# Kernel optimization log

Measured on AMD Instinct MI355X. Metric: run time of the kernel, lower is better.

Reference implementation:

```python
import jax, jax.numpy as jnp
import numpy as np

GAMMA = 1.0
MAX_SIMILARITY = 1.0


def setup_inputs() -> dict:
    key = jax.random.key(0)
    k1, k2 = jax.random.split(key)
    B, Ns, D = 128, 512, 256
    d_vectors = jax.random.normal(k1, (B, Ns, D), dtype=jnp.float32)
    # Normalized similarity matrix (MinMaxScaler output lies in [0, 1])
    S = jax.random.uniform(k2, (Ns, Ns), dtype=jnp.float32)
    return {"d_vectors": d_vectors, "S": S}


def reference(d_vectors, S):
    B, Ns, D = d_vectors.shape
    eye = jnp.eye(Ns, dtype=d_vectors.dtype)

    # Pairwise squared distances: ||di||^2 + ||dj||^2 - 2 di.dj  -> [B, Ns, Ns]
    n2 = jnp.sum(d_vectors * d_vectors, axis=-1)  # [B, Ns]
    sq = n2[:, :, None] + n2[:, None, :] - 2.0 * jnp.einsum("bid,bjd->bij", d_vectors, d_vectors)
    sq = jnp.maximum(sq, 0.0) * (1.0 - eye)  # exact zero on the diagonal

    # Safe sqrt (subgradient 0 at zero distance, matching torch.norm)
    dist = jnp.where(sq > 0, jnp.sqrt(jnp.where(sq > 0, sq, 1.0)), 0.0)
    Kd = jnp.exp(-GAMMA * dist)  # Gaussian-kernel Gram matrix [B, Ns, Ns]

    # Norm-ratio loss
    W = (S > 0).astype(d_vectors.dtype)  # [Ns, Ns]
    denom = jnp.linalg.norm(W - eye)  # Frobenius norm, scalar
    Kd_tilde = Kd * (1.0 - eye)  # zero diagonal
    S_tilde = S - MAX_SIMILARITY * eye
    diff = W * (Kd_tilde - S_tilde)  # broadcast over batch
    numer = jnp.sqrt(jnp.sum(diff * diff, axis=(1, 2)))  # [B]
    losses = 2.0 * numer / denom
    return jnp.sum(losses)
```

## Files before the change

### kernel.cpp

```cpp
#include <hip/hip_runtime.h>
#include <hip/hip_bf16.h>

typedef __bf16 bf16_t;
typedef __bf16 bf16x4 __attribute__((ext_vector_type(4)));
typedef __bf16 bf16x8 __attribute__((ext_vector_type(8)));
typedef float f32x4 __attribute__((ext_vector_type(4)));
typedef float f32x16 __attribute__((ext_vector_type(16)));
typedef long i64x2 __attribute__((ext_vector_type(2)));
typedef int i32x4 __attribute__((ext_vector_type(4)));

#define BATCH 128
#define NS 512
#define DIM 256
#define BT 128
#define NT 10
#define LDSP 272
#define CSTRIDE 132

__global__ __launch_bounds__(256) void prep_st_kernel(const float* __restrict__ dv,
                                                      const float* __restrict__ S,
                                                      unsigned char* __restrict__ f8,
                                                      float* __restrict__ n2g,
                                                      float* __restrict__ St,
                                                      float* __restrict__ dpartial) {
    const int bidx = blockIdx.x;
    const int t = threadIdx.x;
    if (bidx < 256) {
        const int bi = bidx >> 4, bj = bidx & 15;
        const int c  = t & 31, r0 = t >> 5;
        __shared__ float tileS[32][33];
        __shared__ float red[4];
        float dacc = 0.0f;
#pragma unroll
        for (int k = 0; k < 4; ++k) {
            const int r  = r0 + k * 8;
            const int gi = bi * 32 + r, gj = bj * 32 + c;
            const float s = S[(size_t)gi * NS + gj];
            tileS[r][c] = s;
            const float w = (s > 0.0f) ? 1.0f : 0.0f;
            const float e = (gi == gj) ? 1.0f : 0.0f;
            const float d = w - e;
            dacc += d * d;
        }
        __syncthreads();
#pragma unroll
        for (int k = 0; k < 4; ++k) {
            const int r = r0 + k * 8;
            St[(size_t)(bj * 32 + r) * NS + bi * 32 + c] = tileS[c][r];
        }
        const int lane = t & 63, wave = t >> 6;
#pragma unroll
        for (int off = 32; off >= 1; off >>= 1) dacc += __shfl_down(dacc, off, 64);
        if (lane == 0) red[wave] = dacc;
        __syncthreads();
        if (t == 0) dpartial[bidx] = red[0] + red[1] + red[2] + red[3];
    } else {
        const int wid  = ((bidx - 256) << 2) | (t >> 6);
        const int lane = t & 63;
#pragma unroll
        for (int it = 0; it < 8; ++it) {
            const int row = wid + it * 8192;
            const f32x4 v = *reinterpret_cast<const f32x4*>(dv + (size_t)row * DIM + lane * 4);
            float pn = v[0]*v[0] + v[1]*v[1] + v[2]*v[2] + v[3]*v[3];
#pragma unroll
            for (int off = 32; off >= 1; off >>= 1) pn += __shfl_xor(pn, off, 64);
            int w0 = __builtin_amdgcn_cvt_pk_fp8_f32(v[0], v[1], 0, false);
            w0     = __builtin_amdgcn_cvt_pk_fp8_f32(v[2], v[3], w0, true);
            *reinterpret_cast<int*>(f8 + (size_t)row * DIM + lane * 4) = w0;
            if (lane == 0) n2g[row] = pn;
        }
    }
}

__global__ __launch_bounds__(512, 4) void gram_pair_kernel(const unsigned char* __restrict__ f8,
                                                           const float* __restrict__ n2g,
                                                           const float* __restrict__ S,
                                                           const float* __restrict__ St,
                                                           float* __restrict__ partial) {
    const int bid  = blockIdx.x;
    const int work = (bid & 7) * 160 + (bid >> 3);
    const int b    = work / NT;
    const int idx  = work - b * NT;
    int ti, tj;
    if (idx < 4)      { ti = 0; tj = idx; }
    else if (idx < 7) { ti = 1; tj = idx - 3; }
    else if (idx < 9) { ti = 2; tj = idx - 5; }
    else              { ti = 3; tj = 3; }
    const bool diag = (ti == tj);
    const int t    = threadIdx.x;
    const int wave = t >> 6, lane = t & 63;
    const int wr   = wave >> 2, wc = wave & 3;
    const int col  = lane & 31, kh = lane >> 5;

    __shared__ __attribute__((aligned(16))) char smem[256 * LDSP];
    __shared__ float n2s[256];
    __shared__ float red[8];
    char*  sP = smem;
    float* sC = reinterpret_cast<float*>(smem);

    {
        const int g     = t >> 8;
        const int tg    = t & 255;
        const int off16 = (tg & 15) * 16;
        const int rbase = tg >> 4;
        if (g == 0 || !diag) {
            const int psel = g ? tj : ti;
            const unsigned char* src = f8 + ((size_t)b * NS + (size_t)psel * BT) * DIM;
#pragma unroll
            for (int it = 0; it < 8; ++it) {
                const int row = it * 16 + rbase;
                const i32x4 v = *reinterpret_cast<const i32x4*>(src + (size_t)row * DIM + off16);
                *reinterpret_cast<i32x4*>(&sP[(g * 128 + row) * LDSP + off16]) = v;
            }
        }
        if (t < 256) {
            const int p = t >> 7;
            if (p == 0 || !diag) {
                const int psel2 = p ? tj : ti;
                n2s[t] = n2g[(size_t)b * NS + (size_t)psel2 * BT + (t & 127)];
            }
        }
    }
    __syncthreads();

    const int boff = diag ? 0 : 128;
    const char* aP = &sP[(wr * 64 + col) * LDSP + kh * 16];
    const char* bP = &sP[(boff + wc * 32 + col) * LDSP + kh * 16];
    f32x16 acc0 = (f32x16)(0.0f);
    f32x16 acc1 = (f32x16)(0.0f);
    __builtin_amdgcn_s_setprio(1);
#pragma unroll
    for (int u = 0; u < 8; ++u) {
        const i64x2 A0 = *reinterpret_cast<const i64x2*>(aP + u * 32);
        const i64x2 A1 = *reinterpret_cast<const i64x2*>(aP + 32 * LDSP + u * 32);
        const i64x2 Bv = *reinterpret_cast<const i64x2*>(bP + u * 32);
        acc0 = __builtin_amdgcn_mfma_f32_32x32x16_fp8_fp8(A0[0], Bv[0], acc0, 0, 0, 0);
        acc1 = __builtin_amdgcn_mfma_f32_32x32x16_fp8_fp8(A1[0], Bv[0], acc1, 0, 0, 0);
        acc0 = __builtin_amdgcn_mfma_f32_32x32x16_fp8_fp8(A0[1], Bv[1], acc0, 0, 0, 0);
        acc1 = __builtin_amdgcn_mfma_f32_32x32x16_fp8_fp8(A1[1], Bv[1], acc1, 0, 0, 0);
    }
    __builtin_amdgcn_s_setprio(0);
    __syncthreads();

    {
        const int lj = wc * 32 + col;
        const float n2j = n2s[boff + lj];
#pragma unroll
        for (int m = 0; m < 2; ++m) {
            const f32x16 av = m ? acc1 : acc0;
#pragma unroll
            for (int h4 = 0; h4 < 4; ++h4) {
#pragma unroll
                for (int e = 0; e < 4; ++e) {
                    const int li = wr * 64 + m * 32 + h4 * 8 + kh * 4 + e;
                    const float c = av[h4 * 4 + e];
                    const float sq = fmaxf(n2s[li] + n2j - 2.0f * c, 0.0f);
                    sC[li * CSTRIDE + lj] = __expf(-__builtin_amdgcn_sqrtf(sq));
                }
            }
        }
    }
    __syncthreads();

    float local = 0.0f;
    {
        const int rg = t >> 4;
        const int ln = t & 15;
        f32x4 s1a[8], s2a[8];
#pragma unroll
        for (int it = 0; it < 8; ++it) {
            const int li  = rg + (it >> 1) * 32;
            const int ljb = (it & 1) * 64 + ln * 4;
            const int gi  = ti * BT + li;
            s1a[it] = *reinterpret_cast<const f32x4*>(S  + (size_t)gi * NS + tj * BT + ljb);
            s2a[it] = diag ? (f32x4)(0.0f)
                           : *reinterpret_cast<const f32x4*>(St + (size_t)gi * NS + tj * BT + ljb);
        }
#pragma unroll
        for (int it = 0; it < 8; ++it) {
            const int li  = rg + (it >> 1) * 32;
            const int ljb = (it & 1) * 64 + ln * 4;
            const f32x4 kdv = *reinterpret_cast<const f32x4*>(&sC[li * CSTRIDE + ljb]);
#pragma unroll
            for (int e = 0; e < 4; ++e) {
                const int lj = ljb + e;
                const float kd = kdv[e];
                const float s1 = s1a[it][e];
                if (diag) {
                    float d = (li == lj) ? (1.0f - s1) : (kd - s1);
                    d *= (s1 > 0.0f) ? 1.0f : 0.0f;
                    local += d * d;
                } else {
                    const float s2 = s2a[it][e];
                    const float d1 = (s1 > 0.0f) ? (kd - s1) : 0.0f;
                    const float d2 = (s2 > 0.0f) ? (kd - s2) : 0.0f;
                    local += d1 * d1 + d2 * d2;
                }
            }
        }
    }

#pragma unroll
    for (int off = 32; off >= 1; off >>= 1) local += __shfl_down(local, off, 64);
    if (lane == 0) red[wave] = local;
    __syncthreads();
    if (t == 0) {
        float s = 0.0f;
#pragma unroll
        for (int w = 0; w < 8; ++w) s += red[w];
        partial[(size_t)b * NT + idx] = s;
    }
}


__global__ __launch_bounds__(256) void norms_kernel(const float* __restrict__ dv,
                                                    float* __restrict__ n2) {
    const int row  = blockIdx.x * 4 + (threadIdx.x >> 6);
    const int lane = threadIdx.x & 63;
    const float4 v = *reinterpret_cast<const float4*>(dv + (size_t)row * DIM + lane * 4);
    float s = v.x * v.x + v.y * v.y + v.z * v.z + v.w * v.w;
#pragma unroll
    for (int off = 32; off >= 1; off >>= 1) s += __shfl_down(s, off, 64);
    if (lane == 0) n2[row] = s;
}

__global__ __launch_bounds__(256) void denom_kernel(const float* __restrict__ Smat,
                                                    float* __restrict__ dpartial) {
    const int t = threadIdx.x;
    const int lane = t & 63, wave = t >> 6;
    __shared__ float sred[4];
    float acc = 0.0f;
    const int base = blockIdx.x * 512;
#pragma unroll
    for (int r = 0; r < 2; ++r) {
        const int v4 = base + r * 256 + t;
        const float4 s4 = reinterpret_cast<const float4*>(Smat)[v4];
        const int idx0 = v4 * 4;
        const int i = idx0 >> 9;
#pragma unroll
        for (int c = 0; c < 4; ++c) {
            const float s = (&s4.x)[c];
            const int j = (idx0 + c) & (NS - 1);
            const float w = (s > 0.0f) ? 1.0f : 0.0f;
            const float e = (i == j) ? 1.0f : 0.0f;
            const float d = w - e;
            acc += d * d;
        }
    }
#pragma unroll
    for (int off = 32; off >= 1; off >>= 1) acc += __shfl_down(acc, off, 64);
    if (lane == 0) sred[wave] = acc;
    __syncthreads();
    if (t == 0) dpartial[blockIdx.x] = sred[0] + sred[1] + sred[2] + sred[3];
}

#define FLDSK 40
__global__ __launch_bounds__(256) void gram_f32_kernel(const float* __restrict__ dv,
                                                       const float* __restrict__ Smat,
                                                       const float* __restrict__ n2,
                                                       float* __restrict__ partial) {
    const int tile = blockIdx.x;
    const int b    = blockIdx.y;
    const int ti   = tile >> 2, tj = tile & 3;
    const int t    = threadIdx.x;
    const int wave = t >> 6, lane = t & 63;
    const int wr   = wave >> 1, wc = wave & 1;

    __shared__ bf16_t sA[BT * FLDSK];
    __shared__ bf16_t sB[BT * FLDSK];
    __shared__ float red[4];

    const float* Abase = dv + ((size_t)b * NS + (size_t)ti * BT) * DIM;
    const float* Bbase = dv + ((size_t)b * NS + (size_t)tj * BT) * DIM;

    f32x4 acc[4][4];
#pragma unroll
    for (int m = 0; m < 4; ++m)
#pragma unroll
        for (int n = 0; n < 4; ++n) acc[m][n] = (f32x4)(0.0f);

    const int fr = lane & 15;
    const int g  = lane >> 4;

    for (int ks = 0; ks < DIM; ks += 32) {
        float4 ra[4], rb[4];
#pragma unroll
        for (int i = 0; i < 4; ++i) {
            const int c   = i * 256 + t;
            const int row = c >> 3;
            const int kc  = (c & 7) * 4;
            ra[i] = *reinterpret_cast<const float4*>(Abase + (size_t)row * DIM + ks + kc);
            rb[i] = *reinterpret_cast<const float4*>(Bbase + (size_t)row * DIM + ks + kc);
        }
        __syncthreads();
#pragma unroll
        for (int i = 0; i < 4; ++i) {
            const int c   = i * 256 + t;
            const int row = c >> 3;
            const int kc  = (c & 7) * 4;
            bf16x4 va = { (bf16_t)ra[i].x, (bf16_t)ra[i].y, (bf16_t)ra[i].z, (bf16_t)ra[i].w };
            bf16x4 vb = { (bf16_t)rb[i].x, (bf16_t)rb[i].y, (bf16_t)rb[i].z, (bf16_t)rb[i].w };
            *reinterpret_cast<bf16x4*>(&sA[row * FLDSK + kc]) = va;
            *reinterpret_cast<bf16x4*>(&sB[row * FLDSK + kc]) = vb;
        }
        __syncthreads();

        bf16x8 afrag[4], bfrag[4];
#pragma unroll
        for (int m = 0; m < 4; ++m)
            afrag[m] = *reinterpret_cast<const bf16x8*>(&sA[(wr * 64 + m * 16 + fr) * FLDSK + g * 8]);
#pragma unroll
        for (int n = 0; n < 4; ++n)
            bfrag[n] = *reinterpret_cast<const bf16x8*>(&sB[(wc * 64 + n * 16 + fr) * FLDSK + g * 8]);
#pragma unroll
        for (int m = 0; m < 4; ++m)
#pragma unroll
            for (int n = 0; n < 4; ++n)
                acc[m][n] = __builtin_amdgcn_mfma_f32_16x16x32_bf16(afrag[m], bfrag[n], acc[m][n], 0, 0, 0);
    }

    float local = 0.0f;
    const float* n2b = n2 + (size_t)b * NS;
    const int rowbase = ti * BT + wr * 64;
    const int colbase = tj * BT + wc * 64;
#pragma unroll
    for (int m = 0; m < 4; ++m) {
#pragma unroll
        for (int n = 0; n < 4; ++n) {
            const int gi0 = rowbase + m * 16 + g * 4;
            const int gj  = colbase + n * 16 + fr;
            const float ncol = n2b[gj];
#pragma unroll
            for (int j = 0; j < 4; ++j) {
                const int gi = gi0 + j;
                const float cij = acc[m][n][j];
                float sq = fmaxf(n2b[gi] + ncol - 2.0f * cij, 0.0f);
                const float dist = sqrtf(sq);
                const float kd = __expf(-dist);
                const float s = Smat[(size_t)gi * NS + gj];
                const float w = (s > 0.0f) ? 1.0f : 0.0f;
                float d = (gi == gj) ? (1.0f - s) : (kd - s);
                d *= w;
                local += d * d;
            }
        }
    }
#pragma unroll
    for (int off = 32; off >= 1; off >>= 1) local += __shfl_down(local, off, 64);
    if (lane == 0) red[wave] = local;
    __syncthreads();
    if (t == 0) partial[(size_t)b * 16 + tile] = red[0] + red[1] + red[2] + red[3];
}

__global__ __launch_bounds__(256) void finalize_kernel(const float* __restrict__ dpartial, int ndp,
                                                       const float* __restrict__ partial, int ntiles,
                                                       float* __restrict__ out) {
    const int t = threadIdx.x;
    const int lane = t & 63, wave = t >> 6;
    __shared__ float sred[4];
    __shared__ float sred2[4];

    float dacc = (t < ndp) ? dpartial[t] : 0.0f;
#pragma unroll
    for (int off = 32; off >= 1; off >>= 1) dacc += __shfl_down(dacc, off, 64);
    if (lane == 0) sred[wave] = dacc;
    __syncthreads();
    const float denom = sqrtf(sred[0] + sred[1] + sred[2] + sred[3]);

    float lsum = 0.0f;
    if (t < BATCH) {
        float ss = 0.0f;
        for (int k = 0; k < ntiles; ++k) ss += partial[(size_t)t * ntiles + k];
        lsum = 2.0f * sqrtf(ss) / denom;
    }
#pragma unroll
    for (int off = 32; off >= 1; off >>= 1) lsum += __shfl_down(lsum, off, 64);
    if (lane == 0) sred2[wave] = lsum;
    __syncthreads();
    if (t == 0) out[0] = sred2[0] + sred2[1] + sred2[2] + sred2[3];
}

extern "C" void kernel_launch(void* const* d_in, const int* in_sizes, int n_in,
                              void* d_out, int out_size, void* d_ws, size_t ws_size,
                              hipStream_t stream) {
    const float* dv   = (const float*)d_in[0];
    const float* Smat = (const float*)d_in[1];
    float* out = (float*)d_out;

    const size_t f8_bytes = (size_t)BATCH * NS * DIM;
    const size_t st_bytes = (size_t)NS * NS * 4;
    const size_t n2_bytes = (size_t)BATCH * NS * 4;
    const size_t pt_bytes = (size_t)BATCH * 16 * 4;
    const size_t dp_bytes = 256 * 4;
    const size_t need = f8_bytes + st_bytes + n2_bytes + pt_bytes + dp_bytes;

    if (ws_size >= need) {
        char* w = (char*)d_ws;
        unsigned char* f8 = (unsigned char*)w;  w += f8_bytes;
        float* St      = (float*)w;   w += st_bytes;
        float* n2g     = (float*)w;   w += n2_bytes;
        float* partial = (float*)w;   w += pt_bytes;
        float* dpart   = (float*)w;

        prep_st_kernel<<<dim3(2304), 256, 0, stream>>>(dv, Smat, f8, n2g, St, dpart);
        gram_pair_kernel<<<dim3(NT * BATCH), 512, 0, stream>>>(f8, n2g, Smat, St, partial);
        finalize_kernel<<<dim3(1), 256, 0, stream>>>(dpart, 256, partial, NT, out);
    } else {
        float* n2      = (float*)d_ws;
        float* partial = n2 + (size_t)BATCH * NS;
        float* dpart   = partial + (size_t)BATCH * 16;

        norms_kernel<<<dim3(BATCH * NS / 4), 256, 0, stream>>>(dv, n2);
        denom_kernel<<<dim3(128), 256, 0, stream>>>(Smat, dpart);
        gram_f32_kernel<<<dim3(16, BATCH), 256, 0, stream>>>(dv, Smat, n2, partial);
        finalize_kernel<<<dim3(1), 256, 0, stream>>>(dpart, 128, partial, 16, out);
    }
}
```

Before: 45.48 us.

## Split gram tiles into 128x64 half-tiles to double block count and occupancy

Changes the gram_pair work decomposition from 10 symmetric 128x128 tile pairs per batch to 20 rectangular 128x64 tiles. Each block now loads a 128-row A panel and a 64-row B panel, and each wave computes a single 32x32 MFMA accumulator. LDS drops from 256 to 192 rows, and the launch bound asks for 6 blocks per CU instead of 4. The goal is better load balance and latency hiding through more, smaller blocks. The cost is extra A-panel reloads and less MFMA work per wave.

Result: faster. 44.52 us (median of 3 runs) (-2.1%).

```diff
diff --git a/kernel.cpp b/kernel.cpp
--- a/kernel.cpp
+++ b/kernel.cpp
@@ -12,10 +12,9 @@
 #define BATCH 128
 #define NS 512
 #define DIM 256
-#define BT 128
-#define NT 10
+#define NTB 20
 #define LDSP 272
-#define CSTRIDE 132
+#define CST 68
 
 __global__ __launch_bounds__(256) void prep_st_kernel(const float* __restrict__ dv,
                                                       const float* __restrict__ S,
@@ -72,91 +71,75 @@
     }
 }
 
-__global__ __launch_bounds__(512, 4) void gram_pair_kernel(const unsigned char* __restrict__ f8,
+__global__ __launch_bounds__(512, 6) void gram_pair_kernel(const unsigned char* __restrict__ f8,
                                                            const float* __restrict__ n2g,
                                                            const float* __restrict__ S,
                                                            const float* __restrict__ St,
                                                            float* __restrict__ partial) {
     const int bid  = blockIdx.x;
-    const int work = (bid & 7) * 160 + (bid >> 3);
-    const int b    = work / NT;
-    const int idx  = work - b * NT;
-    int ti, tj;
-    if (idx < 4)      { ti = 0; tj = idx; }
-    else if (idx < 7) { ti = 1; tj = idx - 3; }
-    else if (idx < 9) { ti = 2; tj = idx - 5; }
-    else              { ti = 3; tj = 3; }
-    const bool diag = (ti == tj);
+    const int work = (bid & 7) * 320 + (bid >> 3);
+    const int b    = work / NTB;
+    const int r20  = work - b * NTB;
+    int ti, tjc;
+    if (r20 < 8)       { ti = 0; tjc = r20; }
+    else if (r20 < 14) { ti = 1; tjc = r20 - 6; }
+    else if (r20 < 18) { ti = 2; tjc = r20 - 10; }
+    else               { ti = 3; tjc = r20 - 12; }
+    const bool single = ((tjc >> 1) == ti);
     const int t    = threadIdx.x;
     const int wave = t >> 6, lane = t & 63;
-    const int wr   = wave >> 2, wc = wave & 3;
+    const int wr   = wave >> 1, wc = wave & 1;
     const int col  = lane & 31, kh = lane >> 5;
 
-    __shared__ __attribute__((aligned(16))) char smem[256 * LDSP];
-    __shared__ float n2s[256];
+    __shared__ __attribute__((aligned(16))) char smem[192 * LDSP];
+    __shared__ float n2s[192];
     __shared__ float red[8];
     char*  sP = smem;
     float* sC = reinterpret_cast<float*>(smem);
 
     {
-        const int g     = t >> 8;
-        const int tg    = t & 255;
-        const int off16 = (tg & 15) * 16;
-        const int rbase = tg >> 4;
-        if (g == 0 || !diag) {
-            const int psel = g ? tj : ti;
-            const unsigned char* src = f8 + ((size_t)b * NS + (size_t)psel * BT) * DIM;
-#pragma unroll
-            for (int it = 0; it < 8; ++it) {
-                const int row = it * 16 + rbase;
-                const i32x4 v = *reinterpret_cast<const i32x4*>(src + (size_t)row * DIM + off16);
-                *reinterpret_cast<i32x4*>(&sP[(g * 128 + row) * LDSP + off16]) = v;
-            }
-        }
-        if (t < 256) {
-            const int p = t >> 7;
-            if (p == 0 || !diag) {
-                const int psel2 = p ? tj : ti;
-                n2s[t] = n2g[(size_t)b * NS + (size_t)psel2 * BT + (t & 127)];
-            }
-        }
-    }
-    __syncthreads();
-
-    const int boff = diag ? 0 : 128;
-    const char* aP = &sP[(wr * 64 + col) * LDSP + kh * 16];
-    const char* bP = &sP[(boff + wc * 32 + col) * LDSP + kh * 16];
-    f32x16 acc0 = (f32x16)(0.0f);
-    f32x16 acc1 = (f32x16)(0.0f);
+        const unsigned char* srcA = f8 + ((size_t)b * NS + (size_t)ti * 128) * DIM;
+#pragma unroll
+        for (int it = 0; it < 4; ++it) {
+            const i32x4 v = *reinterpret_cast<const i32x4*>(srcA + it * 8192 + t * 16);
+            *reinterpret_cast<i32x4*>(&sP[(it * 32 + (t >> 4)) * LDSP + (t & 15) * 16]) = v;
+        }
+        const unsigned char* srcB = f8 + ((size_t)b * NS + (size_t)tjc * 64) * DIM;
+#pragma unroll
+        for (int it = 0; it < 2; ++it) {
+            const i32x4 v = *reinterpret_cast<const i32x4*>(srcB + it * 8192 + t * 16);
+            *reinterpret_cast<i32x4*>(&sP[(128 + it * 32 + (t >> 4)) * LDSP + (t & 15) * 16]) = v;
+        }
+        if (t < 128)      n2s[t] = n2g[(size_t)b * NS + (size_t)ti * 128 + t];
+        else if (t < 192) n2s[t] = n2g[(size_t)b * NS + (size_t)tjc * 64 + (t - 128)];
+    }
+    __syncthreads();
+
+    const char* aP = &sP[(wr * 32 + col) * LDSP + kh * 16];
+    const char* bP = &sP[(128 + wc * 32 + col) * LDSP + kh * 16];
+    f32x16 acc = (f32x16)(0.0f);
     __builtin_amdgcn_s_setprio(1);
 #pragma unroll
     for (int u = 0; u < 8; ++u) {
-        const i64x2 A0 = *reinterpret_cast<const i64x2*>(aP + u * 32);
-        const i64x2 A1 = *reinterpret_cast<const i64x2*>(aP + 32 * LDSP + u * 32);
+        const i64x2 Av = *reinterpret_cast<const i64x2*>(aP + u * 32);
         const i64x2 Bv = *reinterpret_cast<const i64x2*>(bP + u * 32);
-        acc0 = __builtin_amdgcn_mfma_f32_32x32x16_fp8_fp8(A0[0], Bv[0], acc0, 0, 0, 0);
-        acc1 = __builtin_amdgcn_mfma_f32_32x32x16_fp8_fp8(A1[0], Bv[0], acc1, 0, 0, 0);
-        acc0 = __builtin_amdgcn_mfma_f32_32x32x16_fp8_fp8(A0[1], Bv[1], acc0, 0, 0, 0);
-        acc1 = __builtin_amdgcn_mfma_f32_32x32x16_fp8_fp8(A1[1], Bv[1], acc1, 0, 0, 0);
+        acc = __builtin_amdgcn_mfma_f32_32x32x16_fp8_fp8(Av[0], Bv[0], acc, 0, 0, 0);
+        acc = __builtin_amdgcn_mfma_f32_32x32x16_fp8_fp8(Av[1], Bv[1], acc, 0, 0, 0);
     }
     __builtin_amdgcn_s_setprio(0);
     __syncthreads();
 
     {
         const int lj = wc * 32 + col;
-        const float n2j = n2s[boff + lj];
-#pragma unroll
-        for (int m = 0; m < 2; ++m) {
-            const f32x16 av = m ? acc1 : acc0;
-#pragma unroll
-            for (int h4 = 0; h4 < 4; ++h4) {
-#pragma unroll
-                for (int e = 0; e < 4; ++e) {
-                    const int li = wr * 64 + m * 32 + h4 * 8 + kh * 4 + e;
-                    const float c = av[h4 * 4 + e];
-                    const float sq = fmaxf(n2s[li] + n2j - 2.0f * c, 0.0f);
-                    sC[li * CSTRIDE + lj] = __expf(-__builtin_amdgcn_sqrtf(sq));
-                }
+        const float n2j = n2s[128 + lj];
+#pragma unroll
+        for (int h4 = 0; h4 < 4; ++h4) {
+#pragma unroll
+            for (int e = 0; e < 4; ++e) {
+                const int li = wr * 32 + h4 * 8 + kh * 4 + e;
+                const float c = acc[h4 * 4 + e];
+                const float sq = fmaxf(n2s[li] + n2j - 2.0f * c, 0.0f);
+                sC[li * CST + lj] = __expf(-__builtin_amdgcn_sqrtf(sq));
             }
         }
     }
@@ -166,32 +149,32 @@
     {
         const int rg = t >> 4;
         const int ln = t & 15;
-        f32x4 s1a[8], s2a[8];
-#pragma unroll
-        for (int it = 0; it < 8; ++it) {
-            const int li  = rg + (it >> 1) * 32;
-            const int ljb = (it & 1) * 64 + ln * 4;
-            const int gi  = ti * BT + li;
-            s1a[it] = *reinterpret_cast<const f32x4*>(S  + (size_t)gi * NS + tj * BT + ljb);
-            s2a[it] = diag ? (f32x4)(0.0f)
-                           : *reinterpret_cast<const f32x4*>(St + (size_t)gi * NS + tj * BT + ljb);
-        }
-#pragma unroll
-        for (int it = 0; it < 8; ++it) {
-            const int li  = rg + (it >> 1) * 32;
-            const int ljb = (it & 1) * 64 + ln * 4;
-            const f32x4 kdv = *reinterpret_cast<const f32x4*>(&sC[li * CSTRIDE + ljb]);
+        f32x4 s1a[4], s2a[4];
+#pragma unroll
+        for (int p = 0; p < 4; ++p) {
+            const int li = p * 32 + rg;
+            const int gi = ti * 128 + li;
+            const int cb = tjc * 64 + ln * 4;
+            s1a[p] = *reinterpret_cast<const f32x4*>(S + (size_t)gi * NS + cb);
+            s2a[p] = single ? (f32x4)(0.0f)
+                            : *reinterpret_cast<const f32x4*>(St + (size_t)gi * NS + cb);
+        }
+#pragma unroll
+        for (int p = 0; p < 4; ++p) {
+            const int li = p * 32 + rg;
+            const int gi = ti * 128 + li;
+            const f32x4 kdv = *reinterpret_cast<const f32x4*>(&sC[li * CST + ln * 4]);
 #pragma unroll
             for (int e = 0; e < 4; ++e) {
-                const int lj = ljb + e;
+                const int gj = tjc * 64 + ln * 4 + e;
                 const float kd = kdv[e];
-                const float s1 = s1a[it][e];
-                if (diag) {
-                    float d = (li == lj) ? (1.0f - s1) : (kd - s1);
+                const float s1 = s1a[p][e];
+                if (single) {
+                    float d = (gi == gj) ? (1.0f - s1) : (kd - s1);
                     d *= (s1 > 0.0f) ? 1.0f : 0.0f;
                     local += d * d;
                 } else {
-                    const float s2 = s2a[it][e];
+                    const float s2 = s2a[p][e];
                     const float d1 = (s1 > 0.0f) ? (kd - s1) : 0.0f;
                     const float d2 = (s2 > 0.0f) ? (kd - s2) : 0.0f;
                     local += d1 * d1 + d2 * d2;
@@ -208,7 +191,7 @@
         float s = 0.0f;
 #pragma unroll
         for (int w = 0; w < 8; ++w) s += red[w];
-        partial[(size_t)b * NT + idx] = s;
+        partial[(size_t)b * NTB + r20] = s;
     }
 }
 
@@ -266,12 +249,12 @@
     const int wave = t >> 6, lane = t & 63;
     const int wr   = wave >> 1, wc = wave & 1;
 
-    __shared__ bf16_t sA[BT * FLDSK];
-    __shared__ bf16_t sB[BT * FLDSK];
+    __shared__ bf16_t sA[128 * FLDSK];
+    __shared__ bf16_t sB[128 * FLDSK];
     __shared__ float red[4];
 
-    const float* Abase = dv + ((size_t)b * NS + (size_t)ti * BT) * DIM;
-    const float* Bbase = dv + ((size_t)b * NS + (size_t)tj * BT) * DIM;
+    const float* Abase = dv + ((size_t)b * NS + (size_t)ti * 128) * DIM;
+    const float* Bbase = dv + ((size_t)b * NS + (size_t)tj * 128) * DIM;
 
     f32x4 acc[4][4];
 #pragma unroll
@@ -321,8 +304,8 @@
 
     float local = 0.0f;
     const float* n2b = n2 + (size_t)b * NS;
-    const int rowbase = ti * BT + wr * 64;
-    const int colbase = tj * BT + wc * 64;
+    const int rowbase = ti * 128 + wr * 64;
+    const int colbase = tj * 128 + wc * 64;
 #pragma unroll
     for (int m = 0; m < 4; ++m) {
 #pragma unroll
@@ -390,7 +373,7 @@
     const size_t f8_bytes = (size_t)BATCH * NS * DIM;
     const size_t st_bytes = (size_t)NS * NS * 4;
     const size_t n2_bytes = (size_t)BATCH * NS * 4;
-    const size_t pt_bytes = (size_t)BATCH * 16 * 4;
+    const size_t pt_bytes = (size_t)BATCH * NTB * 4;
     const size_t dp_bytes = 256 * 4;
     const size_t need = f8_bytes + st_bytes + n2_bytes + pt_bytes + dp_bytes;
 
@@ -403,8 +386,8 @@
         float* dpart   = (float*)w;
 
         prep_st_kernel<<<dim3(2304), 256, 0, stream>>>(dv, Smat, f8, n2g, St, dpart);
-        gram_pair_kernel<<<dim3(NT * BATCH), 512, 0, stream>>>(f8, n2g, Smat, St, partial);
-        finalize_kernel<<<dim3(1), 256, 0, stream>>>(dpart, 256, partial, NT, out);
+        gram_pair_kernel<<<dim3(NTB * BATCH), 512, 0, stream>>>(f8, n2g, Smat, St, partial);
+        finalize_kernel<<<dim3(1), 256, 0, stream>>>(dpart, 256, partial, NTB, out);
     } else {
         float* n2      = (float*)d_ws;
         float* partial = n2 + (size_t)BATCH * NS;
```
